# Kernel optimization log

Measured on AMD Instinct MI355X. Metric: run time of the kernel, lower is better.

The kernel has to match this reference:

```python
import jax, jax.numpy as jnp
import numpy as np

EMBED_DIM = 1024
NUM_HEADS = 16
HEAD_DIM = EMBED_DIM // NUM_HEADS
SCALING = HEAD_DIM ** (-0.5)
LN_EPS = 1e-5


def setup_inputs() -> dict:
    key = jax.random.key(0)
    ks = jax.random.split(key, 6)
    N, L, D = 2, 2048, EMBED_DIM
    x = jax.random.normal(ks[0], (N, L, D), dtype=jnp.float32)
    W_in = jax.random.normal(ks[1], (3 * D, D), dtype=jnp.float32) * 0.02
    b_in = jnp.zeros((3 * D,), dtype=jnp.float32)
    Wc = jax.random.normal(ks[2], (HEAD_DIM, HEAD_DIM), dtype=jnp.float32) * 0.1
    bc = jnp.zeros((HEAD_DIM,), dtype=jnp.float32)
    ln_gamma = jnp.ones((HEAD_DIM,), dtype=jnp.float32)
    ln_beta = jnp.zeros((HEAD_DIM,), dtype=jnp.float32)
    W_out = jax.random.normal(ks[3], (D, D), dtype=jnp.float32) * 0.02
    b_out = jnp.zeros((D,), dtype=jnp.float32)
    return {"x": x, "W_in": W_in, "b_in": b_in, "Wc": Wc, "bc": bc,
            "ln_gamma": ln_gamma, "ln_beta": ln_beta, "W_out": W_out, "b_out": b_out}


def _reshape_heads(t, N, L):
    # (N, L, D) -> (N*H, L, head_dim)
    return t.reshape(N, L, NUM_HEADS, HEAD_DIM).transpose(0, 2, 1, 3).reshape(N * NUM_HEADS, L, HEAD_DIM)


def reference(x, W_in, b_in, Wc, bc, ln_gamma, ln_beta, W_out, b_out):
    N, L, D = x.shape
    qkv = jnp.einsum('nld,ed->nle', x, W_in) + b_in  # (N, L, 3D)
    q, k, v = jnp.split(qkv, 3, axis=-1)
    q_head = _reshape_heads(q, N, L)  # (B, L, HD) with B = N*H
    k_head = _reshape_heads(k, N, L)
    v_head = _reshape_heads(v, N, L)

    # Conv1d with kernel_size=1 == pointwise linear on head_dim channels
    q_temp = jnp.einsum('blc,oc->blo', q_head, Wc) + bc
    q_temp = jax.nn.gelu(q_temp, approximate=False)  # torch nn.GELU() is exact erf
    mu = q_temp.mean(axis=-1, keepdims=True)
    var = q_temp.var(axis=-1, keepdims=True)
    q_temp = (q_temp - mu) / jnp.sqrt(var + LN_EPS) * ln_gamma + ln_beta

    q_rel = q_temp.mean(axis=1)  # (B, HD) -- mean over sequence
    # one kernel row per (batch, head): (B, L)
    W_kernel_row = jnp.einsum('bd,bld->bl', q_rel * SCALING, k_head)

    # Toeplitz attention matrix: attn[b, i, j] = W_kernel_row[b, |i-j|]
    idx = jnp.arange(L)
    lags = jnp.abs(idx[:, None] - idx[None, :])  # (L, L), already in [0, L-1]
    attn = W_kernel_row[:, lags]  # (B, L, L) gather

    causal_mask = lags * jnp.sign(idx[None, :] - idx[:, None]) > 0  # j > i
    causal_mask = jnp.triu(jnp.ones((L, L), dtype=bool), k=1)
    attn = jnp.where(causal_mask[None, :, :], -jnp.inf, attn)
    weights = jax.nn.softmax(attn, axis=-1)  # (B, L, L); dropout=0 -> identity

    attn_out = jnp.einsum('bij,bjd->bid', weights, v_head)  # (B, L, HD)
    attn_out = attn_out.reshape(N, NUM_HEADS, L, HEAD_DIM).transpose(0, 2, 1, 3).reshape(N, L, D)
    output = jnp.einsum('nld,ed->nle', attn_out, W_out) + b_out
    return output, weights.mean(axis=1)
```

## Files before the change

### kernel.cpp

```cpp
#include <hip/hip_runtime.h>
#include <math.h>

#define L_SEQ 2048
#define D_EMB 1024
#define NHEADS 16
#define HD 64
#define BHEADS 32
#define NBATCH 2
#define LN_EPS 1e-5f
#define SCALING 0.125f

typedef __attribute__((ext_vector_type(8))) __bf16 bf16x8;
typedef __attribute__((ext_vector_type(4))) float f32x4;
typedef const __attribute__((address_space(1))) unsigned int* gptr_as1;
typedef __attribute__((address_space(3))) unsigned int* lptr_as3;

__device__ __forceinline__ void load16_to_lds(const void* g, void* l) {
  __builtin_amdgcn_global_load_lds((gptr_as1)g, (lptr_as3)l, 16, 0, 0);
}

__device__ __forceinline__ unsigned short f2bf(float f) {
  unsigned int u = __float_as_uint(f);
  u += 0x7fff + ((u >> 16) & 1);
  return (unsigned short)(u >> 16);
}

__device__ __forceinline__ float bf2f(unsigned short us) {
  return __uint_as_float((unsigned int)us << 16);
}

__global__ __launch_bounds__(256) void cvt_bf16_kernel(
    const float* __restrict__ in, unsigned short* __restrict__ out, int n) {
  int i = (blockIdx.x * 256 + threadIdx.x) * 4;
  if (i < n) {
    float4 v = *(const float4*)&in[i];
    ushort4 o;
    o.x = f2bf(v.x); o.y = f2bf(v.y); o.z = f2bf(v.z); o.w = f2bf(v.w);
    *(ushort4*)&out[i] = o;
  }
}

__global__ __launch_bounds__(256) void cvt3_bf16_kernel(
    const float* __restrict__ a, int na, const float* __restrict__ b, int nb,
    const float* __restrict__ c, int nc,
    unsigned short* __restrict__ oa, unsigned short* __restrict__ ob,
    unsigned short* __restrict__ oc) {
  int i = (blockIdx.x * 256 + threadIdx.x) * 4;
  const float* src;
  unsigned short* dst;
  int j;
  if (i < na) { src = a; dst = oa; j = i; }
  else if (i < na + nb) { src = b; dst = ob; j = i - na; }
  else if (i < na + nb + nc) { src = c; dst = oc; j = i - na - nb; }
  else return;
  float4 v = *(const float4*)&src[j];
  ushort4 o;
  o.x = f2bf(v.x); o.y = f2bf(v.y); o.z = f2bf(v.z); o.w = f2bf(v.w);
  *(ushort4*)&dst[j] = o;
}

template<bool QKV>
__global__ __launch_bounds__(256) void gemm_bt32(
    const unsigned short* __restrict__ A, const unsigned short* __restrict__ B,
    const float* __restrict__ bias, void* __restrict__ Cout,
    unsigned short* __restrict__ vT, int M, int Nn, int K) {
  __shared__ unsigned short As[4096];
  __shared__ unsigned short Bs[4096];
  const int bm = blockIdx.y * 128;
  const int bn = blockIdx.x * 128;
  const int tid = threadIdx.x;
  const int lane = tid & 63;
  const int wave = tid >> 6;
  const int wr = (wave >> 1) * 64;
  const int wc = (wave & 1) * 64;

  const int c0 = tid, c1 = tid + 256;
  const unsigned short* ga0 = A + (size_t)(bm + (c0 >> 6) * 16 + (c0 & 15)) * K + ((c0 >> 4) & 3) * 8;
  const unsigned short* ga1 = A + (size_t)(bm + (c1 >> 6) * 16 + (c1 & 15)) * K + ((c1 >> 4) & 3) * 8;
  const unsigned short* gb0 = B + (size_t)(bn + (c0 >> 6) * 16 + (c0 & 15)) * K + ((c0 >> 4) & 3) * 8;
  const unsigned short* gb1 = B + (size_t)(bn + (c1 >> 6) * 16 + (c1 & 15)) * K + ((c1 >> 4) & 3) * 8;

  f32x4 acc[4][4] = {};
  for (int k0 = 0; k0 < K; k0 += 32) {
    load16_to_lds(ga0 + k0, &As[c0 * 8]);
    load16_to_lds(ga1 + k0, &As[c1 * 8]);
    load16_to_lds(gb0 + k0, &Bs[c0 * 8]);
    load16_to_lds(gb1 + k0, &Bs[c1 * 8]);
    __syncthreads();
    bf16x8 af[4], bf[4];
    #pragma unroll
    for (int i = 0; i < 4; ++i)
      af[i] = *(const bf16x8*)&As[((wr >> 4) + i) * 512 + lane * 8];
    #pragma unroll
    for (int j = 0; j < 4; ++j)
      bf[j] = *(const bf16x8*)&Bs[((wc >> 4) + j) * 512 + lane * 8];
    #pragma unroll
    for (int i = 0; i < 4; ++i)
      #pragma unroll
      for (int j = 0; j < 4; ++j)
        acc[i][j] = __builtin_amdgcn_mfma_f32_16x16x32_bf16(af[i], bf[j], acc[i][j], 0, 0, 0);
    __syncthreads();
  }
  const int lc = lane & 15;
  const int lr4 = (lane >> 4) << 2;
  float bv[4];
  #pragma unroll
  for (int j = 0; j < 4; ++j) bv[j] = bias[bn + wc + j * 16 + lc];
  if (!QKV) {
    float* C = (float*)Cout;
    #pragma unroll
    for (int i = 0; i < 4; ++i)
      #pragma unroll
      for (int r = 0; r < 4; ++r) {
        const int row = bm + wr + i * 16 + lr4 + r;
        float* cp = &C[(size_t)row * Nn + bn + wc + lc];
        #pragma unroll
        for (int j = 0; j < 4; ++j) cp[j * 16] = acc[i][j][r] + bv[j];
      }
  } else if (bn < 2 * D_EMB) {
    unsigned short* C = (unsigned short*)Cout;
    #pragma unroll
    for (int i = 0; i < 4; ++i)
      #pragma unroll
      for (int r = 0; r < 4; ++r) {
        const int row = bm + wr + i * 16 + lr4 + r;
        unsigned short* cp = &C[(size_t)row * Nn + bn + wc + lc];
        #pragma unroll
        for (int j = 0; j < 4; ++j) cp[j * 16] = f2bf(acc[i][j][r] + bv[j]);
      }
  } else {
    #pragma unroll
    for (int i = 0; i < 4; ++i) {
      const int row0 = bm + wr + i * 16 + lr4;
      const int n = row0 >> 11;
      const int jseq = row0 & (L_SEQ - 1);
      #pragma unroll
      for (int j = 0; j < 4; ++j) {
        const int col = bn + wc + j * 16 + lc;
        const int d = col & 63;
        const int h = (col >> 6) & 15;
        ushort4 o;
        o.x = f2bf(acc[i][j][0] + bv[j]);
        o.y = f2bf(acc[i][j][1] + bv[j]);
        o.z = f2bf(acc[i][j][2] + bv[j]);
        o.w = f2bf(acc[i][j][3] + bv[j]);
        *(ushort4*)&vT[(size_t)((n * 16 + h) * 64 + d) * L_SEQ + jseq] = o;
      }
    }
  }
}

__global__ __launch_bounds__(256) void qtemp_mfma_kernel(
    const unsigned short* __restrict__ qkv_bf, const unsigned short* __restrict__ Wc_bf,
    const float* __restrict__ bc, const float* __restrict__ gamma,
    const float* __restrict__ beta, float* __restrict__ q_rel_sum) {
  __shared__ unsigned short Qs[16384];
  __shared__ unsigned short Ws[4096];
  __shared__ float red[4][64];
  const int b = blockIdx.y;
  const int n = b >> 4, h = b & 15;
  const int l0 = blockIdx.x * 256;
  const int tid = threadIdx.x;
  const int lane = tid & 63;
  const int wave = tid >> 6;
  const int quad = lane >> 4;
  const int mi = lane & 15;

  #pragma unroll
  for (int s = 0; s < 8; ++s) {
    const int c = tid + s * 256;
    const int row = ((c >> 7) << 4) + (c & 15);
    const int kof = ((c >> 4) & 7) << 3;
    load16_to_lds(qkv_bf + (size_t)(n * L_SEQ + l0 + row) * (3 * D_EMB) + h * 64 + kof,
                  &Qs[c * 8]);
  }
  #pragma unroll
  for (int s = 0; s < 2; ++s) {
    const int c = tid + s * 256;
    const int row = ((c >> 7) << 4) + (c & 15);
    const int kof = ((c >> 4) & 7) << 3;
    load16_to_lds(Wc_bf + row * 64 + kof, &Ws[c * 8]);
  }
  __syncthreads();

  f32x4 acc[4][4] = {};
  #pragma unroll
  for (int kk = 0; kk < 2; ++kk) {
    const int fo = ((kk * 4 + quad) * 16 + mi) * 8;
    bf16x8 bf[4];
    #pragma unroll
    for (int t = 0; t < 4; ++t) bf[t] = *(const bf16x8*)&Ws[t * 1024 + fo];
    #pragma unroll
    for (int isub = 0; isub < 4; ++isub) {
      const bf16x8 af = *(const bf16x8*)&Qs[(wave * 4 + isub) * 1024 + fo];
      #pragma unroll
      for (int t = 0; t < 4; ++t)
        acc[isub][t] = __builtin_amdgcn_mfma_f32_16x16x32_bf16(af, bf[t], acc[isub][t], 0, 0, 0);
    }
  }

  float bcv[4], gav[4], bev[4], colacc[4];
  #pragma unroll
  for (int t = 0; t < 4; ++t) {
    const int col = t * 16 + mi;
    bcv[t] = bc[col]; gav[t] = gamma[col]; bev[t] = beta[col];
    colacc[t] = 0.f;
  }
  #pragma unroll
  for (int isub = 0; isub < 4; ++isub) {
    #pragma unroll
    for (int r = 0; r < 4; ++r) {
      float g[4];
      float s1 = 0.f, s2 = 0.f;
      #pragma unroll
      for (int t = 0; t < 4; ++t) {
        const float d = acc[isub][t][r] + bcv[t];
        const float gg = 0.5f * d * (1.f + erff(d * 0.70710678118654752f));
        g[t] = gg;
        s1 += gg;
        s2 += gg * gg;
      }
      #pragma unroll
      for (int off = 8; off > 0; off >>= 1) {
        s1 += __shfl_xor(s1, off);
        s2 += __shfl_xor(s2, off);
      }
      const float mu = s1 * (1.f / 64.f);
      const float var = s2 * (1.f / 64.f) - mu * mu;
      const float rs = rsqrtf(var + LN_EPS);
      #pragma unroll
      for (int t = 0; t < 4; ++t)
        colacc[t] += (g[t] - mu) * rs * gav[t] + bev[t];
    }
  }
  #pragma unroll
  for (int t = 0; t < 4; ++t) {
    colacc[t] += __shfl_xor(colacc[t], 16);
    colacc[t] += __shfl_xor(colacc[t], 32);
  }
  if (quad == 0) {
    #pragma unroll
    for (int t = 0; t < 4; ++t) red[wave][t * 16 + mi] = colacc[t];
  }
  __syncthreads();
  if (wave == 0) {
    float tot = red[0][lane] + red[1][lane] + red[2][lane] + red[3][lane];
    atomicAdd(&q_rel_sum[b * 64 + lane], tot);
  }
}

__global__ __launch_bounds__(256) void wrow_kernel(
    const unsigned short* __restrict__ qkv_bf, const float* __restrict__ q_rel_sum,
    float* __restrict__ w_row) {
  const int b = blockIdx.x;
  const int n = b >> 4, h = b & 15;
  __shared__ float q_s[64];
  const int tid = threadIdx.x;
  if (tid < 64) q_s[tid] = q_rel_sum[b * 64 + tid] * (SCALING / (float)L_SEQ);
  __syncthreads();
  const int t = blockIdx.y * 256 + tid;
  const unsigned short* kp = &qkv_bf[(size_t)(n * L_SEQ + t) * (3 * D_EMB) + D_EMB + h * 64];
  float acc = 0.f;
  #pragma unroll
  for (int c = 0; c < 64; c += 8) {
    uint4 kv = *(const uint4*)&kp[c];
    acc += q_s[c + 0] * __uint_as_float(kv.x << 16);
    acc += q_s[c + 1] * __uint_as_float(kv.x & 0xffff0000u);
    acc += q_s[c + 2] * __uint_as_float(kv.y << 16);
    acc += q_s[c + 3] * __uint_as_float(kv.y & 0xffff0000u);
    acc += q_s[c + 4] * __uint_as_float(kv.z << 16);
    acc += q_s[c + 5] * __uint_as_float(kv.z & 0xffff0000u);
    acc += q_s[c + 6] * __uint_as_float(kv.w << 16);
    acc += q_s[c + 7] * __uint_as_float(kv.w & 0xffff0000u);
  }
  w_row[b * L_SEQ + t] = acc;
}

__global__ __launch_bounds__(256) void scan_kernel(
    const float* __restrict__ w_row, float* __restrict__ e_out,
    float* __restrict__ inv_out) {
  const int b = blockIdx.x;
  const int tid = threadIdx.x;
  __shared__ float sh[L_SEQ];
  __shared__ float ts[256];
  const float* wb = w_row + b * L_SEQ;
  float m = -3.4e38f;
  for (int i = tid; i < L_SEQ; i += 256) {
    float v = wb[i];
    sh[i] = v;
    m = fmaxf(m, v);
  }
  ts[tid] = m;
  __syncthreads();
  for (int off = 128; off > 0; off >>= 1) {
    if (tid < off) ts[tid] = fmaxf(ts[tid], ts[tid + off]);
    __syncthreads();
  }
  const float mx = ts[0];
  __syncthreads();
  const int t0 = tid * 8;
  float loc[8];
  float run = 0.f;
  #pragma unroll
  for (int k = 0; k < 8; ++k) {
    float ev = expf(sh[t0 + k] - mx);
    e_out[b * L_SEQ + t0 + k] = ev;
    run += ev;
    loc[k] = run;
  }
  ts[tid] = run;
  __syncthreads();
  for (int off = 1; off < 256; off <<= 1) {
    float v = ts[tid];
    float add = (tid >= off) ? ts[tid - off] : 0.f;
    __syncthreads();
    ts[tid] = v + add;
    __syncthreads();
  }
  float prefix = (tid > 0) ? ts[tid - 1] : 0.f;
  #pragma unroll
  for (int k = 0; k < 8; ++k)
    inv_out[b * L_SEQ + t0 + k] = 1.f / (prefix + loc[k]);
}

__global__ __launch_bounds__(256) void conv_mfma_kernel(
    const unsigned short* __restrict__ vT, const float* __restrict__ e_arr,
    const float* __restrict__ inv_arr, unsigned short* __restrict__ attn_out) {
  __shared__ unsigned short V_s[2][4096];
  __shared__ unsigned short rep[2][8 * 320];
  const int blk = 7 - blockIdx.x;
  const int b = blockIdx.y;
  const int n = b >> 4, h = b & 15;
  const int blkI = blk * 256;
  const int blk4 = blk * 4;
  const int njt = blk4 + 4;
  const int tid = threadIdx.x;
  const int lane = tid & 63;
  const int wave = tid >> 6;
  const int quad = lane >> 4;
  const int mi = lane & 15;
  const float* e_b = e_arr + b * L_SEQ;

  const int c0 = tid, c1 = tid + 256;
  const unsigned short* vsrc0 = vT + (size_t)(b * 64 + (c0 >> 7) * 16 + (c0 & 15)) * L_SEQ + ((c0 >> 4) & 7) * 8;
  const unsigned short* vsrc1 = vT + (size_t)(b * 64 + (c1 >> 7) * 16 + (c1 & 15)) * L_SEQ + ((c1 >> 4) & 7) * 8;

  f32x4 acc[4][4] = {};

  {
    load16_to_lds(vsrc0, &V_s[0][c0 * 8]);
    load16_to_lds(vsrc1, &V_s[0][c1 * 8]);
    const int lagBase = blkI;
    int v = tid;
    int lag = lagBase + 256 - v;
    float ev = (lag >= 0 && lag < L_SEQ) ? e_b[lag] : 0.f;
    unsigned short bfv = f2bf(ev);
    #pragma unroll
    for (int r = 0; r < 8; ++r) { int idx = v - r; if (idx >= 0) rep[0][r * 320 + idx] = bfv; }
    if (tid < 64) {
      v = tid + 256;
      lag = lagBase - tid;
      ev = (lag >= 0 && lag < L_SEQ) ? e_b[lag] : 0.f;
      bfv = f2bf(ev);
      #pragma unroll
      for (int r = 0; r < 8; ++r) rep[0][r * 320 + (v - r)] = bfv;
    }
  }

  for (int jt = 0; jt < njt; ++jt) {
    __syncthreads();
    const int cb = jt & 1;
    if (jt + 1 < njt) {
      const int pb = cb ^ 1;
      const int j0 = (jt + 1) * 64;
      load16_to_lds(vsrc0 + j0, &V_s[pb][c0 * 8]);
      load16_to_lds(vsrc1 + j0, &V_s[pb][c1 * 8]);
      const int lagBase = blkI - j0;
      int v = tid;
      int lag = lagBase + 256 - v;
      float ev = (lag >= 0 && lag < L_SEQ) ? e_b[lag] : 0.f;
      unsigned short bfv = f2bf(ev);
      #pragma unroll
      for (int r = 0; r < 8; ++r) { int idx = v - r; if (idx >= 0) rep[pb][r * 320 + idx] = bfv; }
      if (tid < 64) {
        v = tid + 256;
        lag = lagBase - tid;
        ev = (lag >= 0 && lag < L_SEQ) ? e_b[lag] : 0.f;
        bfv = f2bf(ev);
        #pragma unroll
        for (int r = 0; r < 8; ++r) rep[pb][r * 320 + (v - r)] = bfv;
      }
    }
    if (jt <= blk4 + wave) {
      const unsigned short* Vb = V_s[cb];
      const unsigned short* Rb = rep[cb];
      bf16x8 ef[6];
      #pragma unroll
      for (int q = 0; q < 6; ++q) {
        const int s = 256 - wave * 64 - mi + quad * 8 - 16 * (q - 2);
        const int rr = s & 7;
        ef[q] = *(const bf16x8*)&Rb[rr * 320 + (s - rr)];
      }
      #pragma unroll
      for (int kk = 0; kk < 2; ++kk) {
        bf16x8 bv[4];
        #pragma unroll
        for (int t = 0; t < 4; ++t)
          bv[t] = *(const bf16x8*)&Vb[t * 1024 + kk * 512 + lane * 8];
        #pragma unroll
        for (int isub = 0; isub < 4; ++isub) {
          const int qi = isub - 2 * kk + 2;
          #pragma unroll
          for (int t = 0; t < 4; ++t)
            acc[isub][t] = __builtin_amdgcn_mfma_f32_16x16x32_bf16(ef[qi], bv[t], acc[isub][t], 0, 0, 0);
        }
      }
    }
  }
  #pragma unroll
  for (int isub = 0; isub < 4; ++isub) {
    #pragma unroll
    for (int r = 0; r < 4; ++r) {
      const int i = blkI + wave * 64 + isub * 16 + quad * 4 + r;
      const float iv = inv_arr[b * L_SEQ + i];
      unsigned short* op = &attn_out[((size_t)(n * L_SEQ + i)) * D_EMB + h * 64 + mi];
      #pragma unroll
      for (int t = 0; t < 4; ++t) op[t * 16] = f2bf(acc[isub][t][r] * iv);
    }
  }
}

__global__ __launch_bounds__(256) void wmean_kernel(
    const float* __restrict__ e_arr, const float* __restrict__ inv_arr,
    float* __restrict__ out_wm) {
  const int b = blockIdx.x;
  __shared__ float e_s[L_SEQ];
  __shared__ float inv_s[L_SEQ];
  __shared__ float red[256];
  const int tid = threadIdx.x;
  for (int i = tid; i < L_SEQ; i += 256) {
    e_s[i] = e_arr[b * L_SEQ + i];
    inv_s[i] = inv_arr[b * L_SEQ + i];
  }
  __syncthreads();
  const int jj = tid & 127;
  const int h2 = tid >> 7;
  const int j = blockIdx.y * 128 + jj;
  float acc = 0.f;
  for (int d = h2; j + d < L_SEQ; d += 2) acc += e_s[d] * inv_s[j + d];
  red[tid] = acc;
  __syncthreads();
  if (tid < 128)
    out_wm[b * L_SEQ + j] = (red[tid] + red[tid + 128]) * (1.f / (float)L_SEQ);
}

extern "C" void kernel_launch(void* const* d_in, const int* in_sizes, int n_in,
                              void* d_out, int out_size, void* d_ws, size_t ws_size,
                              hipStream_t stream) {
  const float* x       = (const float*)d_in[0];
  const float* W_in    = (const float*)d_in[1];
  const float* b_in    = (const float*)d_in[2];
  const float* Wc      = (const float*)d_in[3];
  const float* bc      = (const float*)d_in[4];
  const float* gamma   = (const float*)d_in[5];
  const float* beta    = (const float*)d_in[6];
  const float* W_out   = (const float*)d_in[7];
  const float* b_out   = (const float*)d_in[8];
  float* out = (float*)d_out;

  const int M = NBATCH * L_SEQ;
  char* ws = (char*)d_ws;
  unsigned short* xa_bf  = (unsigned short*)ws;
  unsigned short* Win_bf = (unsigned short*)(ws + 8388608);
  unsigned short* Wout_bf= (unsigned short*)(ws + 14680064);
  unsigned short* qkv_bf = (unsigned short*)(ws + 16777216);
  unsigned short* vT     = (unsigned short*)(ws + 41943040);
  float* q_rel = (float*)(ws + 50331648);
  float* e_arr = (float*)(ws + 50339840);
  float* inv_a = (float*)(ws + 50601984);
  float* w_row = (float*)(ws + 50864128);
  unsigned short* Wc_bf  = (unsigned short*)(ws + 51126272);

  hipMemsetAsync(q_rel, 0, BHEADS * HD * sizeof(float), stream);

  cvt_bf16_kernel<<<dim3(M * D_EMB / 1024), 256, 0, stream>>>(x, xa_bf, M * D_EMB);
  cvt3_bf16_kernel<<<dim3((3 * D_EMB * D_EMB + D_EMB * D_EMB + HD * HD) / 1024), 256, 0, stream>>>(
      W_in, 3 * D_EMB * D_EMB, W_out, D_EMB * D_EMB, Wc, HD * HD, Win_bf, Wout_bf, Wc_bf);
  gemm_bt32<true><<<dim3(3 * D_EMB / 128, M / 128), 256, 0, stream>>>(
      xa_bf, Win_bf, b_in, qkv_bf, vT, M, 3 * D_EMB, D_EMB);
  qtemp_mfma_kernel<<<dim3(8, BHEADS), 256, 0, stream>>>(
      qkv_bf, Wc_bf, bc, gamma, beta, q_rel);
  wrow_kernel<<<dim3(BHEADS, 8), 256, 0, stream>>>(qkv_bf, q_rel, w_row);
  scan_kernel<<<dim3(BHEADS), 256, 0, stream>>>(w_row, e_arr, inv_a);
  conv_mfma_kernel<<<dim3(8, BHEADS), 256, 0, stream>>>(vT, e_arr, inv_a, xa_bf);
  wmean_kernel<<<dim3(BHEADS, L_SEQ / 128), 256, 0, stream>>>(
      e_arr, inv_a, out + (size_t)M * D_EMB);
  gemm_bt32<false><<<dim3(D_EMB / 128, M / 128), 256, 0, stream>>>(
      xa_bf, Wout_bf, b_out, out, nullptr, M, D_EMB, D_EMB);
}
```

Before: 297.2 us.

## Raise grid parallelism across conv, qtemp and output GEMM; merge conversion launches

Splits the conv kernel along head dimension into two z-blocks and halves the qtemp tile, giving more blocks per launch. The output projection GEMM moves to a 64-row tile, which doubles the block count for better CU occupancy. The QKV GEMM gains a remapped block order for L2 locality, and the x conversion is folded into a single four-way conversion launch. The trade-off is more redundant work in conv (the lag-replication buffer is rebuilt per half) and less operand reuse per block in the GEMM.

```diff
diff --git a/kernel.cpp b/kernel.cpp
--- a/kernel.cpp
+++ b/kernel.cpp
@@ -25,26 +25,11 @@
   return (unsigned short)(u >> 16);
 }
 
-__device__ __forceinline__ float bf2f(unsigned short us) {
-  return __uint_as_float((unsigned int)us << 16);
-}
-
-__global__ __launch_bounds__(256) void cvt_bf16_kernel(
-    const float* __restrict__ in, unsigned short* __restrict__ out, int n) {
-  int i = (blockIdx.x * 256 + threadIdx.x) * 4;
-  if (i < n) {
-    float4 v = *(const float4*)&in[i];
-    ushort4 o;
-    o.x = f2bf(v.x); o.y = f2bf(v.y); o.z = f2bf(v.z); o.w = f2bf(v.w);
-    *(ushort4*)&out[i] = o;
-  }
-}
-
-__global__ __launch_bounds__(256) void cvt3_bf16_kernel(
+__global__ __launch_bounds__(256) void cvt4_bf16_kernel(
     const float* __restrict__ a, int na, const float* __restrict__ b, int nb,
-    const float* __restrict__ c, int nc,
+    const float* __restrict__ c, int nc, const float* __restrict__ d, int nd,
     unsigned short* __restrict__ oa, unsigned short* __restrict__ ob,
-    unsigned short* __restrict__ oc) {
+    unsigned short* __restrict__ oc, unsigned short* __restrict__ od) {
   int i = (blockIdx.x * 256 + threadIdx.x) * 4;
   const float* src;
   unsigned short* dst;
@@ -52,6 +37,7 @@
   if (i < na) { src = a; dst = oa; j = i; }
   else if (i < na + nb) { src = b; dst = ob; j = i - na; }
   else if (i < na + nb + nc) { src = c; dst = oc; j = i - na - nb; }
+  else if (i < na + nb + nc + nd) { src = d; dst = od; j = i - na - nb - nc; }
   else return;
   float4 v = *(const float4*)&src[j];
   ushort4 o;
@@ -59,15 +45,17 @@
   *(ushort4*)&dst[j] = o;
 }
 
-template<bool QKV>
-__global__ __launch_bounds__(256) void gemm_bt32(
+__global__ __launch_bounds__(256) void gemm_qkv(
     const unsigned short* __restrict__ A, const unsigned short* __restrict__ B,
-    const float* __restrict__ bias, void* __restrict__ Cout,
+    const float* __restrict__ bias, unsigned short* __restrict__ Cbf,
     unsigned short* __restrict__ vT, int M, int Nn, int K) {
   __shared__ unsigned short As[4096];
   __shared__ unsigned short Bs[4096];
-  const int bm = blockIdx.y * 128;
-  const int bn = blockIdx.x * 128;
+  const int id = blockIdx.y * 24 + blockIdx.x;
+  const int by = (id / 48) * 2 + (id & 1);
+  const int bx = (id % 48) >> 1;
+  const int bm = by * 128;
+  const int bn = bx * 128;
   const int tid = threadIdx.x;
   const int lane = tid & 63;
   const int wave = tid >> 6;
@@ -106,25 +94,13 @@
   float bv[4];
   #pragma unroll
   for (int j = 0; j < 4; ++j) bv[j] = bias[bn + wc + j * 16 + lc];
-  if (!QKV) {
-    float* C = (float*)Cout;
+  if (bn < 2 * D_EMB) {
     #pragma unroll
     for (int i = 0; i < 4; ++i)
       #pragma unroll
       for (int r = 0; r < 4; ++r) {
         const int row = bm + wr + i * 16 + lr4 + r;
-        float* cp = &C[(size_t)row * Nn + bn + wc + lc];
-        #pragma unroll
-        for (int j = 0; j < 4; ++j) cp[j * 16] = acc[i][j][r] + bv[j];
-      }
-  } else if (bn < 2 * D_EMB) {
-    unsigned short* C = (unsigned short*)Cout;
-    #pragma unroll
-    for (int i = 0; i < 4; ++i)
-      #pragma unroll
-      for (int r = 0; r < 4; ++r) {
-        const int row = bm + wr + i * 16 + lr4 + r;
-        unsigned short* cp = &C[(size_t)row * Nn + bn + wc + lc];
+        unsigned short* cp = &Cbf[(size_t)row * Nn + bn + wc + lc];
         #pragma unroll
         for (int j = 0; j < 4; ++j) cp[j * 16] = f2bf(acc[i][j][r] + bv[j]);
       }
@@ -150,16 +126,72 @@
   }
 }
 
+__global__ __launch_bounds__(256) void gemm_out64(
+    const unsigned short* __restrict__ A, const unsigned short* __restrict__ B,
+    const float* __restrict__ bias, float* __restrict__ C,
+    int M, int Nn, int K) {
+  __shared__ unsigned short As[2048];
+  __shared__ unsigned short Bs[4096];
+  const int bm = blockIdx.y * 64;
+  const int bn = blockIdx.x * 128;
+  const int tid = threadIdx.x;
+  const int lane = tid & 63;
+  const int wave = tid >> 6;
+  const int wr = (wave >> 1) * 32;
+  const int wc = (wave & 1) * 64;
+
+  const int ca = tid;
+  const int cb0 = tid, cb1 = tid + 256;
+  const unsigned short* ga = A + (size_t)(bm + (ca >> 6) * 16 + (ca & 15)) * K + ((ca >> 4) & 3) * 8;
+  const unsigned short* gb0 = B + (size_t)(bn + (cb0 >> 6) * 16 + (cb0 & 15)) * K + ((cb0 >> 4) & 3) * 8;
+  const unsigned short* gb1 = B + (size_t)(bn + (cb1 >> 6) * 16 + (cb1 & 15)) * K + ((cb1 >> 4) & 3) * 8;
+
+  f32x4 acc[2][4] = {};
+  for (int k0 = 0; k0 < K; k0 += 32) {
+    load16_to_lds(ga + k0, &As[ca * 8]);
+    load16_to_lds(gb0 + k0, &Bs[cb0 * 8]);
+    load16_to_lds(gb1 + k0, &Bs[cb1 * 8]);
+    __syncthreads();
+    bf16x8 af[2], bf[4];
+    #pragma unroll
+    for (int i = 0; i < 2; ++i)
+      af[i] = *(const bf16x8*)&As[((wr >> 4) + i) * 512 + lane * 8];
+    #pragma unroll
+    for (int j = 0; j < 4; ++j)
+      bf[j] = *(const bf16x8*)&Bs[((wc >> 4) + j) * 512 + lane * 8];
+    #pragma unroll
+    for (int i = 0; i < 2; ++i)
+      #pragma unroll
+      for (int j = 0; j < 4; ++j)
+        acc[i][j] = __builtin_amdgcn_mfma_f32_16x16x32_bf16(af[i], bf[j], acc[i][j], 0, 0, 0);
+    __syncthreads();
+  }
+  const int lc = lane & 15;
+  const int lr4 = (lane >> 4) << 2;
+  float bv[4];
+  #pragma unroll
+  for (int j = 0; j < 4; ++j) bv[j] = bias[bn + wc + j * 16 + lc];
+  #pragma unroll
+  for (int i = 0; i < 2; ++i)
+    #pragma unroll
+    for (int r = 0; r < 4; ++r) {
+      const int row = bm + wr + i * 16 + lr4 + r;
+      float* cp = &C[(size_t)row * Nn + bn + wc + lc];
+      #pragma unroll
+      for (int j = 0; j < 4; ++j) cp[j * 16] = acc[i][j][r] + bv[j];
+    }
+}
+
 __global__ __launch_bounds__(256) void qtemp_mfma_kernel(
     const unsigned short* __restrict__ qkv_bf, const unsigned short* __restrict__ Wc_bf,
     const float* __restrict__ bc, const float* __restrict__ gamma,
     const float* __restrict__ beta, float* __restrict__ q_rel_sum) {
-  __shared__ unsigned short Qs[16384];
+  __shared__ unsigned short Qs[8192];
   __shared__ unsigned short Ws[4096];
   __shared__ float red[4][64];
   const int b = blockIdx.y;
   const int n = b >> 4, h = b & 15;
-  const int l0 = blockIdx.x * 256;
+  const int l0 = blockIdx.x * 128;
   const int tid = threadIdx.x;
   const int lane = tid & 63;
   const int wave = tid >> 6;
@@ -167,7 +199,7 @@
   const int mi = lane & 15;
 
   #pragma unroll
-  for (int s = 0; s < 8; ++s) {
+  for (int s = 0; s < 4; ++s) {
     const int c = tid + s * 256;
     const int row = ((c >> 7) << 4) + (c & 15);
     const int kof = ((c >> 4) & 7) << 3;
@@ -183,7 +215,7 @@
   }
   __syncthreads();
 
-  f32x4 acc[4][4] = {};
+  f32x4 acc[2][4] = {};
   #pragma unroll
   for (int kk = 0; kk < 2; ++kk) {
     const int fo = ((kk * 4 + quad) * 16 + mi) * 8;
@@ -191,8 +223,8 @@
     #pragma unroll
     for (int t = 0; t < 4; ++t) bf[t] = *(const bf16x8*)&Ws[t * 1024 + fo];
     #pragma unroll
-    for (int isub = 0; isub < 4; ++isub) {
-      const bf16x8 af = *(const bf16x8*)&Qs[(wave * 4 + isub) * 1024 + fo];
+    for (int isub = 0; isub < 2; ++isub) {
+      const bf16x8 af = *(const bf16x8*)&Qs[(wave * 2 + isub) * 1024 + fo];
       #pragma unroll
       for (int t = 0; t < 4; ++t)
         acc[isub][t] = __builtin_amdgcn_mfma_f32_16x16x32_bf16(af, bf[t], acc[isub][t], 0, 0, 0);
@@ -207,7 +239,7 @@
     colacc[t] = 0.f;
   }
   #pragma unroll
-  for (int isub = 0; isub < 4; ++isub) {
+  for (int isub = 0; isub < 2; ++isub) {
     #pragma unroll
     for (int r = 0; r < 4; ++r) {
       float g[4];
@@ -326,10 +358,11 @@
 __global__ __launch_bounds__(256) void conv_mfma_kernel(
     const unsigned short* __restrict__ vT, const float* __restrict__ e_arr,
     const float* __restrict__ inv_arr, unsigned short* __restrict__ attn_out) {
-  __shared__ unsigned short V_s[2][4096];
+  __shared__ unsigned short V_s[2][2048];
   __shared__ unsigned short rep[2][8 * 320];
   const int blk = 7 - blockIdx.x;
   const int b = blockIdx.y;
+  const int dh = blockIdx.z;
   const int n = b >> 4, h = b & 15;
   const int blkI = blk * 256;
   const int blk4 = blk * 4;
@@ -341,15 +374,13 @@
   const int mi = lane & 15;
   const float* e_b = e_arr + b * L_SEQ;
 
-  const int c0 = tid, c1 = tid + 256;
-  const unsigned short* vsrc0 = vT + (size_t)(b * 64 + (c0 >> 7) * 16 + (c0 & 15)) * L_SEQ + ((c0 >> 4) & 7) * 8;
-  const unsigned short* vsrc1 = vT + (size_t)(b * 64 + (c1 >> 7) * 16 + (c1 & 15)) * L_SEQ + ((c1 >> 4) & 7) * 8;
-
-  f32x4 acc[4][4] = {};
+  const unsigned short* vsrc = vT +
+      (size_t)(b * 64 + dh * 32 + (tid >> 7) * 16 + (tid & 15)) * L_SEQ + ((tid >> 4) & 7) * 8;
+
+  f32x4 acc[4][2] = {};
 
   {
-    load16_to_lds(vsrc0, &V_s[0][c0 * 8]);
-    load16_to_lds(vsrc1, &V_s[0][c1 * 8]);
+    load16_to_lds(vsrc, &V_s[0][tid * 8]);
     const int lagBase = blkI;
     int v = tid;
     int lag = lagBase + 256 - v;
@@ -373,8 +404,7 @@
     if (jt + 1 < njt) {
       const int pb = cb ^ 1;
       const int j0 = (jt + 1) * 64;
-      load16_to_lds(vsrc0 + j0, &V_s[pb][c0 * 8]);
-      load16_to_lds(vsrc1 + j0, &V_s[pb][c1 * 8]);
+      load16_to_lds(vsrc + j0, &V_s[pb][tid * 8]);
       const int lagBase = blkI - j0;
       int v = tid;
       int lag = lagBase + 256 - v;
@@ -403,15 +433,15 @@
       }
       #pragma unroll
       for (int kk = 0; kk < 2; ++kk) {
-        bf16x8 bv[4];
+        bf16x8 bv[2];
         #pragma unroll
-        for (int t = 0; t < 4; ++t)
+        for (int t = 0; t < 2; ++t)
           bv[t] = *(const bf16x8*)&Vb[t * 1024 + kk * 512 + lane * 8];
         #pragma unroll
         for (int isub = 0; isub < 4; ++isub) {
           const int qi = isub - 2 * kk + 2;
           #pragma unroll
-          for (int t = 0; t < 4; ++t)
+          for (int t = 0; t < 2; ++t)
             acc[isub][t] = __builtin_amdgcn_mfma_f32_16x16x32_bf16(ef[qi], bv[t], acc[isub][t], 0, 0, 0);
         }
       }
@@ -423,9 +453,9 @@
     for (int r = 0; r < 4; ++r) {
       const int i = blkI + wave * 64 + isub * 16 + quad * 4 + r;
       const float iv = inv_arr[b * L_SEQ + i];
-      unsigned short* op = &attn_out[((size_t)(n * L_SEQ + i)) * D_EMB + h * 64 + mi];
-      #pragma unroll
-      for (int t = 0; t < 4; ++t) op[t * 16] = f2bf(acc[isub][t][r] * iv);
+      unsigned short* op = &attn_out[((size_t)(n * L_SEQ + i)) * D_EMB + h * 64 + dh * 32 + mi];
+      #pragma unroll
+      for (int t = 0; t < 2; ++t) op[t * 16] = f2bf(acc[isub][t][r] * iv);
     }
   }
 }
@@ -483,18 +513,20 @@
 
   hipMemsetAsync(q_rel, 0, BHEADS * HD * sizeof(float), stream);
 
-  cvt_bf16_kernel<<<dim3(M * D_EMB / 1024), 256, 0, stream>>>(x, xa_bf, M * D_EMB);
-  cvt3_bf16_kernel<<<dim3((3 * D_EMB * D_EMB + D_EMB * D_EMB + HD * HD) / 1024), 256, 0, stream>>>(
-      W_in, 3 * D_EMB * D_EMB, W_out, D_EMB * D_EMB, Wc, HD * HD, Win_bf, Wout_bf, Wc_bf);
-  gemm_bt32<true><<<dim3(3 * D_EMB / 128, M / 128), 256, 0, stream>>>(
+  {
+    const int na = M * D_EMB, nb = 3 * D_EMB * D_EMB, nc = D_EMB * D_EMB, nd = HD * HD;
+    cvt4_bf16_kernel<<<dim3((na + nb + nc + nd) / 1024), 256, 0, stream>>>(
+        x, na, W_in, nb, W_out, nc, Wc, nd, xa_bf, Win_bf, Wout_bf, Wc_bf);
+  }
+  gemm_qkv<<<dim3(24, 32), 256, 0, stream>>>(
       xa_bf, Win_bf, b_in, qkv_bf, vT, M, 3 * D_EMB, D_EMB);
-  qtemp_mfma_kernel<<<dim3(8, BHEADS), 256, 0, stream>>>(
+  qtemp_mfma_kernel<<<dim3(16, BHEADS), 256, 0, stream>>>(
       qkv_bf, Wc_bf, bc, gamma, beta, q_rel);
   wrow_kernel<<<dim3(BHEADS, 8), 256, 0, stream>>>(qkv_bf, q_rel, w_row);
   scan_kernel<<<dim3(BHEADS), 256, 0, stream>>>(w_row, e_arr, inv_a);
-  conv_mfma_kernel<<<dim3(8, BHEADS), 256, 0, stream>>>(vT, e_arr, inv_a, xa_bf);
   wmean_kernel<<<dim3(BHEADS, L_SEQ / 128), 256, 0, stream>>>(
       e_arr, inv_a, out + (size_t)M * D_EMB);
-  gemm_bt32<false><<<dim3(D_EMB / 128, M / 128), 256, 0, stream>>>(
-      xa_bf, Wout_bf, b_out, out, nullptr, M, D_EMB, D_EMB);
-}
+  conv_mfma_kernel<<<dim3(8, BHEADS, 2), 256, 0, stream>>>(vT, e_arr, inv_a, xa_bf);
+  gemm_out64<<<dim3(D_EMB / 128, M / 64), 256, 0, stream>>>(
+      xa_bf, Wout_bf, b_out, out, M, D_EMB, D_EMB);
+}
```

Result: faster. 277.4 us (-6.7%).
